# Kernel optimization log

Measured on AMD Instinct MI355X. Metric: run time of the kernel, lower is better.

Reference implementation:

```python
import jax, jax.numpy as jnp
import numpy as np


def setup_inputs() -> dict:
    key = jax.random.key(0)
    k1, = jax.random.split(key, 1)
    b, l, h, w, c = 2, 16, 16, 16, 32
    inputs = jax.random.normal(k1, (b, l, h, w, c), dtype=jnp.float32)
    gamma = jnp.ones((1,), dtype=jnp.float32)
    return {"inputs": inputs, "gamma": gamma}


def reference(inputs, gamma):
    b, l, h, w, c = inputs.shape
    n = l * h * w
    # torch: x = permute->view gives [b, c, n]; here keep [b, n, c] (same memory layout of values)
    xr = inputs.reshape(b, n, c)
    # scores[b,i,j] = sum_c x[b,c,i] * x[b,c,j]
    scores = jnp.einsum('bic,bjc->bij', xr, xr)
    attn = jax.nn.softmax(scores, axis=-1)  # softmax over j (dim=-1)
    # out[b,c,j] = sum_i x[b,c,i] * attn[b,i,j]  ->  [b, n, c] layout
    out = jnp.einsum('bic,bij->bjc', xr, attn)
    out = out.reshape(b, l, h, w, c)
    return out * gamma + inputs
```

## Files before the change

kernel.cpp:

```cpp
#include <hip/hip_runtime.h>


typedef _Float16 half8 __attribute__((ext_vector_type(8)));
typedef _Float16 half4v __attribute__((ext_vector_type(4)));
typedef _Float16 half2v __attribute__((ext_vector_type(2)));
typedef float float4v __attribute__((ext_vector_type(4)));
typedef int int4v __attribute__((ext_vector_type(4)));

#define NN 4096
#define CC 32
#define L2E 1.44269504f
#define SHIFT 48.0f

__global__ __launch_bounds__(256) void k_convert(const float* __restrict__ x,
                                                 _Float16* __restrict__ xf,
                                                 _Float16* __restrict__ xt) {
    const int t = blockIdx.x * 256 + threadIdx.x;
    const int n  = t & 4095;
    const int cg = (t >> 12) & 7;
    const int b  = t >> 15;
    const int row = (b << 12) | n;
    const float4* src = (const float4*)(x + (size_t)row * CC + cg * 4);
    float4 v = *src;
    _Float16 h0 = (_Float16)v.x, h1 = (_Float16)v.y, h2 = (_Float16)v.z, h3 = (_Float16)v.w;
    *(half4v*)(xf + (size_t)row * CC + cg * 4) = (half4v){h0, h1, h2, h3};
    _Float16* p = xt + (size_t)b * CC * NN + (size_t)(n >> 5) * (CC * 32) + cg * 4 * 32 + (n & 31);
    p[0]  = h0;
    p[32] = h1;
    p[64] = h2;
    p[96] = h3;
}

__global__ __launch_bounds__(512, 2) void k_pass1(const _Float16* __restrict__ xf,
                                                  float* __restrict__ c2out) {
    const int tid = threadIdx.x;
    const int wave = tid >> 6, lane = tid & 63;
    const int quad = lane >> 4, l15 = lane & 15;
    const int b = blockIdx.x >> 6;
    const int i0 = (blockIdx.x & 63) * 64;
    const _Float16* xb = xf + (size_t)b * NN * CC;

    const half8 af0 = *(const half8*)(xb + (size_t)(i0 + l15) * CC + quad * 8);
    const half8 af1 = *(const half8*)(xb + (size_t)(i0 + 16 + l15) * CC + quad * 8);
    const half8 af2 = *(const half8*)(xb + (size_t)(i0 + 32 + l15) * CC + quad * 8);
    const half8 af3 = *(const half8*)(xb + (size_t)(i0 + 48 + l15) * CC + quad * 8);
    const float4v zf = {0.f, 0.f, 0.f, 0.f};
    float z0[4] = {0.f, 0.f, 0.f, 0.f};
    float z1[4] = {0.f, 0.f, 0.f, 0.f};
    float z2[4] = {0.f, 0.f, 0.f, 0.f};
    float z3[4] = {0.f, 0.f, 0.f, 0.f};
    const float c2c = -SHIFT * L2E;

    const int jbase = wave * 512;
    half8 b0 = *(const half8*)(xb + (size_t)(jbase + l15) * CC + quad * 8);
    half8 b1 = *(const half8*)(xb + (size_t)(jbase + 16 + l15) * CC + quad * 8);
    half8 b2 = *(const half8*)(xb + (size_t)(jbase + 32 + l15) * CC + quad * 8);
    half8 b3 = *(const half8*)(xb + (size_t)(jbase + 48 + l15) * CC + quad * 8);

    for (int jt = 0; jt < 8; ++jt) {
        const int jn = jbase + ((jt + 1) & 7) * 64;
        half8 n0 = *(const half8*)(xb + (size_t)(jn + l15) * CC + quad * 8);
        half8 n1 = *(const half8*)(xb + (size_t)(jn + 16 + l15) * CC + quad * 8);
        half8 n2 = *(const half8*)(xb + (size_t)(jn + 32 + l15) * CC + quad * 8);
        half8 n3 = *(const half8*)(xb + (size_t)(jn + 48 + l15) * CC + quad * 8);

        {
            float4v s00 = __builtin_amdgcn_mfma_f32_16x16x32_f16(af0, b0, zf, 0, 0, 0);
            float4v s01 = __builtin_amdgcn_mfma_f32_16x16x32_f16(af0, b1, zf, 0, 0, 0);
            float4v s02 = __builtin_amdgcn_mfma_f32_16x16x32_f16(af0, b2, zf, 0, 0, 0);
            float4v s03 = __builtin_amdgcn_mfma_f32_16x16x32_f16(af0, b3, zf, 0, 0, 0);
            float4v s10 = __builtin_amdgcn_mfma_f32_16x16x32_f16(af1, b0, zf, 0, 0, 0);
            float4v s11 = __builtin_amdgcn_mfma_f32_16x16x32_f16(af1, b1, zf, 0, 0, 0);
            float4v s12 = __builtin_amdgcn_mfma_f32_16x16x32_f16(af1, b2, zf, 0, 0, 0);
            float4v s13 = __builtin_amdgcn_mfma_f32_16x16x32_f16(af1, b3, zf, 0, 0, 0);
#pragma unroll
            for (int r = 0; r < 4; ++r) {
                z0[r] += __builtin_amdgcn_exp2f(fmaf(s00[r], L2E, c2c));
                z0[r] += __builtin_amdgcn_exp2f(fmaf(s01[r], L2E, c2c));
                z0[r] += __builtin_amdgcn_exp2f(fmaf(s02[r], L2E, c2c));
                z0[r] += __builtin_amdgcn_exp2f(fmaf(s03[r], L2E, c2c));
                z1[r] += __builtin_amdgcn_exp2f(fmaf(s10[r], L2E, c2c));
                z1[r] += __builtin_amdgcn_exp2f(fmaf(s11[r], L2E, c2c));
                z1[r] += __builtin_amdgcn_exp2f(fmaf(s12[r], L2E, c2c));
                z1[r] += __builtin_amdgcn_exp2f(fmaf(s13[r], L2E, c2c));
            }
        }
        {
            float4v s00 = __builtin_amdgcn_mfma_f32_16x16x32_f16(af2, b0, zf, 0, 0, 0);
            float4v s01 = __builtin_amdgcn_mfma_f32_16x16x32_f16(af2, b1, zf, 0, 0, 0);
            float4v s02 = __builtin_amdgcn_mfma_f32_16x16x32_f16(af2, b2, zf, 0, 0, 0);
            float4v s03 = __builtin_amdgcn_mfma_f32_16x16x32_f16(af2, b3, zf, 0, 0, 0);
            float4v s10 = __builtin_amdgcn_mfma_f32_16x16x32_f16(af3, b0, zf, 0, 0, 0);
            float4v s11 = __builtin_amdgcn_mfma_f32_16x16x32_f16(af3, b1, zf, 0, 0, 0);
            float4v s12 = __builtin_amdgcn_mfma_f32_16x16x32_f16(af3, b2, zf, 0, 0, 0);
            float4v s13 = __builtin_amdgcn_mfma_f32_16x16x32_f16(af3, b3, zf, 0, 0, 0);
#pragma unroll
            for (int r = 0; r < 4; ++r) {
                z2[r] += __builtin_amdgcn_exp2f(fmaf(s00[r], L2E, c2c));
                z2[r] += __builtin_amdgcn_exp2f(fmaf(s01[r], L2E, c2c));
                z2[r] += __builtin_amdgcn_exp2f(fmaf(s02[r], L2E, c2c));
                z2[r] += __builtin_amdgcn_exp2f(fmaf(s03[r], L2E, c2c));
                z3[r] += __builtin_amdgcn_exp2f(fmaf(s10[r], L2E, c2c));
                z3[r] += __builtin_amdgcn_exp2f(fmaf(s11[r], L2E, c2c));
                z3[r] += __builtin_amdgcn_exp2f(fmaf(s12[r], L2E, c2c));
                z3[r] += __builtin_amdgcn_exp2f(fmaf(s13[r], L2E, c2c));
            }
        }
        b0 = n0; b1 = n1; b2 = n2; b3 = n3;
    }
#pragma unroll
    for (int off = 1; off <= 8; off <<= 1) {
#pragma unroll
        for (int r = 0; r < 4; ++r) {
            z0[r] += __shfl_xor(z0[r], off, 64);
            z1[r] += __shfl_xor(z1[r], off, 64);
            z2[r] += __shfl_xor(z2[r], off, 64);
            z3[r] += __shfl_xor(z3[r], off, 64);
        }
    }
    __shared__ float zw[8][64];
    if (l15 == 0) {
#pragma unroll
        for (int r = 0; r < 4; ++r) {
            zw[wave][quad * 4 + r]      = z0[r];
            zw[wave][16 + quad * 4 + r] = z1[r];
            zw[wave][32 + quad * 4 + r] = z2[r];
            zw[wave][48 + quad * 4 + r] = z3[r];
        }
    }
    __syncthreads();
    if (tid < 64) {
        float zs = 0.f;
#pragma unroll
        for (int w = 0; w < 8; ++w) zs += zw[w][tid];
        c2out[b * NN + i0 + tid] = -(__builtin_amdgcn_logf(zs) + SHIFT * L2E);
    }
}

__global__ __launch_bounds__(512, 2) void k_pass2(const _Float16* __restrict__ xf,
                                                  const _Float16* __restrict__ xt,
                                                  const float* __restrict__ c2,
                                                  const float* __restrict__ x,
                                                  const float* __restrict__ gamma,
                                                  float* __restrict__ out) {
    const int tid = threadIdx.x;
    const int wave = tid >> 6, lane = tid & 63;
    const int quad = lane >> 4, l15 = lane & 15;
    const int b = blockIdx.x >> 6;
    const int j0 = (blockIdx.x & 63) * 64;
    const _Float16* xb  = xf + (size_t)b * NN * CC;
    const _Float16* xtb = xt + (size_t)b * CC * NN;
    const float* c2b = c2 + b * NN;

    __shared__ float red[8][64][32];

    const int addrLo = (((quad & 1) << 5) + l15) << 2;
    const int addrHi = addrLo + 64;
    const bool lo32 = (lane < 32);

    const half8 bj0 = *(const half8*)(xb + (size_t)(j0 + l15) * CC + quad * 8);
    const half8 bj1 = *(const half8*)(xb + (size_t)(j0 + 16 + l15) * CC + quad * 8);
    const half8 bj2 = *(const half8*)(xb + (size_t)(j0 + 32 + l15) * CC + quad * 8);
    const half8 bj3 = *(const half8*)(xb + (size_t)(j0 + 48 + l15) * CC + quad * 8);
    const float4v zf = {0.f, 0.f, 0.f, 0.f};
    float4v acc00 = zf, acc01 = zf, acc10 = zf, acc11 = zf;
    float4v acc20 = zf, acc21 = zf, acc30 = zf, acc31 = zf;

    const int ibase = wave * 512;
    half8 a0  = *(const half8*)(xb + (size_t)(ibase + l15) * CC + quad * 8);
    half8 a1  = *(const half8*)(xb + (size_t)(ibase + 16 + l15) * CC + quad * 8);
    half8 xb0 = *(const half8*)(xtb + (size_t)ibase * 32 + l15 * 32 + quad * 8);
    half8 xb1 = *(const half8*)(xtb + (size_t)ibase * 32 + 512 + l15 * 32 + quad * 8);
    float4v c20 = *(const float4v*)(c2b + ibase + quad * 4);
    float4v c21 = *(const float4v*)(c2b + ibase + 16 + quad * 4);

    for (int it = 0; it < 16; ++it) {
        const int inx = ibase + ((it + 1) & 15) * 32;
        half8 na0  = *(const half8*)(xb + (size_t)(inx + l15) * CC + quad * 8);
        half8 na1  = *(const half8*)(xb + (size_t)(inx + 16 + l15) * CC + quad * 8);
        half8 nxb0 = *(const half8*)(xtb + (size_t)inx * 32 + l15 * 32 + quad * 8);
        half8 nxb1 = *(const half8*)(xtb + (size_t)inx * 32 + 512 + l15 * 32 + quad * 8);
        float4v nc20 = *(const float4v*)(c2b + inx + quad * 4);
        float4v nc21 = *(const float4v*)(c2b + inx + 16 + quad * 4);

        {
            float4v s00 = __builtin_amdgcn_mfma_f32_16x16x32_f16(a0, bj0, zf, 0, 0, 0);
            float4v s10 = __builtin_amdgcn_mfma_f32_16x16x32_f16(a1, bj0, zf, 0, 0, 0);
            float4v s01 = __builtin_amdgcn_mfma_f32_16x16x32_f16(a0, bj1, zf, 0, 0, 0);
            float4v s11 = __builtin_amdgcn_mfma_f32_16x16x32_f16(a1, bj1, zf, 0, 0, 0);
            float4v e00, e10, e01, e11;
#pragma unroll
            for (int r = 0; r < 4; ++r) {
                e00[r] = __builtin_amdgcn_exp2f(fmaf(s00[r], L2E, c20[r]));
                e10[r] = __builtin_amdgcn_exp2f(fmaf(s10[r], L2E, c21[r]));
                e01[r] = __builtin_amdgcn_exp2f(fmaf(s01[r], L2E, c20[r]));
                e11[r] = __builtin_amdgcn_exp2f(fmaf(s11[r], L2E, c21[r]));
            }
            {
                const int d0 = __builtin_bit_cast(int, (half2v)__builtin_amdgcn_cvt_pkrtz(e00[0], e00[1]));
                const int d1 = __builtin_bit_cast(int, (half2v)__builtin_amdgcn_cvt_pkrtz(e00[2], e00[3]));
                const int d2 = __builtin_bit_cast(int, (half2v)__builtin_amdgcn_cvt_pkrtz(e10[0], e10[1]));
                const int d3 = __builtin_bit_cast(int, (half2v)__builtin_amdgcn_cvt_pkrtz(e10[2], e10[3]));
                const int q0 = __builtin_amdgcn_ds_bpermute(addrLo, d0);
                const int q1 = __builtin_amdgcn_ds_bpermute(addrLo, d1);
                const int q2 = __builtin_amdgcn_ds_bpermute(addrHi, d0);
                const int q3 = __builtin_amdgcn_ds_bpermute(addrHi, d1);
                const int q4 = __builtin_amdgcn_ds_bpermute(addrLo, d2);
                const int q5 = __builtin_amdgcn_ds_bpermute(addrLo, d3);
                const int q6 = __builtin_amdgcn_ds_bpermute(addrHi, d2);
                const int q7 = __builtin_amdgcn_ds_bpermute(addrHi, d3);
                int4v ai;
                ai[0] = lo32 ? q0 : q4;
                ai[1] = lo32 ? q1 : q5;
                ai[2] = lo32 ? q2 : q6;
                ai[3] = lo32 ? q3 : q7;
                const half8 a2 = __builtin_bit_cast(half8, ai);
                acc00 = __builtin_amdgcn_mfma_f32_16x16x32_f16(a2, xb0, acc00, 0, 0, 0);
                acc01 = __builtin_amdgcn_mfma_f32_16x16x32_f16(a2, xb1, acc01, 0, 0, 0);
            }
            {
                const int d0 = __builtin_bit_cast(int, (half2v)__builtin_amdgcn_cvt_pkrtz(e01[0], e01[1]));
                const int d1 = __builtin_bit_cast(int, (half2v)__builtin_amdgcn_cvt_pkrtz(e01[2], e01[3]));
                const int d2 = __builtin_bit_cast(int, (half2v)__builtin_amdgcn_cvt_pkrtz(e11[0], e11[1]));
                const int d3 = __builtin_bit_cast(int, (half2v)__builtin_amdgcn_cvt_pkrtz(e11[2], e11[3]));
                const int q0 = __builtin_amdgcn_ds_bpermute(addrLo, d0);
                const int q1 = __builtin_amdgcn_ds_bpermute(addrLo, d1);
                const int q2 = __builtin_amdgcn_ds_bpermute(addrHi, d0);
                const int q3 = __builtin_amdgcn_ds_bpermute(addrHi, d1);
                const int q4 = __builtin_amdgcn_ds_bpermute(addrLo, d2);
                const int q5 = __builtin_amdgcn_ds_bpermute(addrLo, d3);
                const int q6 = __builtin_amdgcn_ds_bpermute(addrHi, d2);
                const int q7 = __builtin_amdgcn_ds_bpermute(addrHi, d3);
                int4v ai;
                ai[0] = lo32 ? q0 : q4;
                ai[1] = lo32 ? q1 : q5;
                ai[2] = lo32 ? q2 : q6;
                ai[3] = lo32 ? q3 : q7;
                const half8 a2 = __builtin_bit_cast(half8, ai);
                acc10 = __builtin_amdgcn_mfma_f32_16x16x32_f16(a2, xb0, acc10, 0, 0, 0);
                acc11 = __builtin_amdgcn_mfma_f32_16x16x32_f16(a2, xb1, acc11, 0, 0, 0);
            }
        }
        {
            float4v s00 = __builtin_amdgcn_mfma_f32_16x16x32_f16(a0, bj2, zf, 0, 0, 0);
            float4v s10 = __builtin_amdgcn_mfma_f32_16x16x32_f16(a1, bj2, zf, 0, 0, 0);
            float4v s01 = __builtin_amdgcn_mfma_f32_16x16x32_f16(a0, bj3, zf, 0, 0, 0);
            float4v s11 = __builtin_amdgcn_mfma_f32_16x16x32_f16(a1, bj3, zf, 0, 0, 0);
            float4v e00, e10, e01, e11;
#pragma unroll
            for (int r = 0; r < 4; ++r) {
                e00[r] = __builtin_amdgcn_exp2f(fmaf(s00[r], L2E, c20[r]));
                e10[r] = __builtin_amdgcn_exp2f(fmaf(s10[r], L2E, c21[r]));
                e01[r] = __builtin_amdgcn_exp2f(fmaf(s01[r], L2E, c20[r]));
                e11[r] = __builtin_amdgcn_exp2f(fmaf(s11[r], L2E, c21[r]));
            }
            {
                const int d0 = __builtin_bit_cast(int, (half2v)__builtin_amdgcn_cvt_pkrtz(e00[0], e00[1]));
                const int d1 = __builtin_bit_cast(int, (half2v)__builtin_amdgcn_cvt_pkrtz(e00[2], e00[3]));
                const int d2 = __builtin_bit_cast(int, (half2v)__builtin_amdgcn_cvt_pkrtz(e10[0], e10[1]));
                const int d3 = __builtin_bit_cast(int, (half2v)__builtin_amdgcn_cvt_pkrtz(e10[2], e10[3]));
                const int q0 = __builtin_amdgcn_ds_bpermute(addrLo, d0);
                const int q1 = __builtin_amdgcn_ds_bpermute(addrLo, d1);
                const int q2 = __builtin_amdgcn_ds_bpermute(addrHi, d0);
                const int q3 = __builtin_amdgcn_ds_bpermute(addrHi, d1);
                const int q4 = __builtin_amdgcn_ds_bpermute(addrLo, d2);
                const int q5 = __builtin_amdgcn_ds_bpermute(addrLo, d3);
                const int q6 = __builtin_amdgcn_ds_bpermute(addrHi, d2);
                const int q7 = __builtin_amdgcn_ds_bpermute(addrHi, d3);
                int4v ai;
                ai[0] = lo32 ? q0 : q4;
                ai[1] = lo32 ? q1 : q5;
                ai[2] = lo32 ? q2 : q6;
                ai[3] = lo32 ? q3 : q7;
                const half8 a2 = __builtin_bit_cast(half8, ai);
                acc20 = __builtin_amdgcn_mfma_f32_16x16x32_f16(a2, xb0, acc20, 0, 0, 0);
                acc21 = __builtin_amdgcn_mfma_f32_16x16x32_f16(a2, xb1, acc21, 0, 0, 0);
            }
            {
                const int d0 = __builtin_bit_cast(int, (half2v)__builtin_amdgcn_cvt_pkrtz(e01[0], e01[1]));
                const int d1 = __builtin_bit_cast(int, (half2v)__builtin_amdgcn_cvt_pkrtz(e01[2], e01[3]));
                const int d2 = __builtin_bit_cast(int, (half2v)__builtin_amdgcn_cvt_pkrtz(e11[0], e11[1]));
                const int d3 = __builtin_bit_cast(int, (half2v)__builtin_amdgcn_cvt_pkrtz(e11[2], e11[3]));
                const int q0 = __builtin_amdgcn_ds_bpermute(addrLo, d0);
                const int q1 = __builtin_amdgcn_ds_bpermute(addrLo, d1);
                const int q2 = __builtin_amdgcn_ds_bpermute(addrHi, d0);
                const int q3 = __builtin_amdgcn_ds_bpermute(addrHi, d1);
                const int q4 = __builtin_amdgcn_ds_bpermute(addrLo, d2);
                const int q5 = __builtin_amdgcn_ds_bpermute(addrLo, d3);
                const int q6 = __builtin_amdgcn_ds_bpermute(addrHi, d2);
                const int q7 = __builtin_amdgcn_ds_bpermute(addrHi, d3);
                int4v ai;
                ai[0] = lo32 ? q0 : q4;
                ai[1] = lo32 ? q1 : q5;
                ai[2] = lo32 ? q2 : q6;
                ai[3] = lo32 ? q3 : q7;
                const half8 a2 = __builtin_bit_cast(half8, ai);
                acc30 = __builtin_amdgcn_mfma_f32_16x16x32_f16(a2, xb0, acc30, 0, 0, 0);
                acc31 = __builtin_amdgcn_mfma_f32_16x16x32_f16(a2, xb1, acc31, 0, 0, 0);
            }
        }

        a0 = na0; a1 = na1; xb0 = nxb0; xb1 = nxb1; c20 = nc20; c21 = nc21;
    }

#pragma unroll
    for (int r = 0; r < 4; ++r) {
        red[wave][quad * 4 + r][l15]           = acc00[r];
        red[wave][quad * 4 + r][l15 + 16]      = acc01[r];
        red[wave][16 + quad * 4 + r][l15]      = acc10[r];
        red[wave][16 + quad * 4 + r][l15 + 16] = acc11[r];
        red[wave][32 + quad * 4 + r][l15]      = acc20[r];
        red[wave][32 + quad * 4 + r][l15 + 16] = acc21[r];
        red[wave][48 + quad * 4 + r][l15]      = acc30[r];
        red[wave][48 + quad * 4 + r][l15 + 16] = acc31[r];
    }
    __syncthreads();
    {
        const int jj = tid >> 5, c = tid & 31;
        const float g = gamma[0];
#pragma unroll
        for (int h = 0; h < 4; ++h) {
            const int j = jj + h * 16;
            float s = 0.f;
#pragma unroll
            for (int w = 0; w < 8; ++w) s += red[w][j][c];
            const size_t o = (size_t)(b * NN + j0 + j) * CC + c;
            out[o] = fmaf(g, s, x[o]);
        }
    }
}

extern "C" void kernel_launch(void* const* d_in, const int* in_sizes, int n_in,
                              void* d_out, int out_size, void* d_ws, size_t ws_size,
                              hipStream_t stream) {
    const float* x     = (const float*)d_in[0];
    const float* gamma = (const float*)d_in[1];
    float* out = (float*)d_out;

    _Float16* xf = (_Float16*)d_ws;
    _Float16* xt = xf + (size_t)2 * NN * CC;
    float*    c2 = (float*)(xt + (size_t)2 * CC * NN);

    k_convert<<<dim3(256), dim3(256), 0, stream>>>(x, xf, xt);
    k_pass1 <<<dim3(128), dim3(512), 0, stream>>>(xf, c2);
    k_pass2 <<<dim3(128), dim3(512), 0, stream>>>(xf, xt, c2, x, gamma, out);
}
```

Baseline: 87.49 us.

## Double grid size by splitting query rows in pass1 and i-range in pass2

Pass1 now gives each block 32 query rows instead of 64, doubling its grid to 256 blocks. Pass2 splits the i-reduction into two halves across 256 blocks and combines the partial outputs with float atomicAdd into an output zeroed by the convert kernel, with the residual added by one half only. The aim is to fill more of the GPU's compute units, since 128 blocks underuse the device. The cost is atomic traffic, an extra zeroing write, and a summation order that depends on atomic timing.

```diff
diff --git a/kernel.cpp b/kernel.cpp
--- a/kernel.cpp
+++ b/kernel.cpp
@@ -14,7 +14,8 @@
 
 __global__ __launch_bounds__(256) void k_convert(const float* __restrict__ x,
                                                  _Float16* __restrict__ xf,
-                                                 _Float16* __restrict__ xt) {
+                                                 _Float16* __restrict__ xt,
+                                                 float* __restrict__ out) {
     const int t = blockIdx.x * 256 + threadIdx.x;
     const int n  = t & 4095;
     const int cg = (t >> 12) & 7;
@@ -29,6 +30,7 @@
     p[32] = h1;
     p[64] = h2;
     p[96] = h3;
+    *(float4*)(out + (size_t)t * 4) = (float4){0.f, 0.f, 0.f, 0.f};
 }
 
 __global__ __launch_bounds__(512, 2) void k_pass1(const _Float16* __restrict__ xf,
@@ -36,19 +38,15 @@
     const int tid = threadIdx.x;
     const int wave = tid >> 6, lane = tid & 63;
     const int quad = lane >> 4, l15 = lane & 15;
-    const int b = blockIdx.x >> 6;
-    const int i0 = (blockIdx.x & 63) * 64;
+    const int b = blockIdx.x >> 7;
+    const int i0 = (blockIdx.x & 127) * 32;
     const _Float16* xb = xf + (size_t)b * NN * CC;
 
     const half8 af0 = *(const half8*)(xb + (size_t)(i0 + l15) * CC + quad * 8);
     const half8 af1 = *(const half8*)(xb + (size_t)(i0 + 16 + l15) * CC + quad * 8);
-    const half8 af2 = *(const half8*)(xb + (size_t)(i0 + 32 + l15) * CC + quad * 8);
-    const half8 af3 = *(const half8*)(xb + (size_t)(i0 + 48 + l15) * CC + quad * 8);
     const float4v zf = {0.f, 0.f, 0.f, 0.f};
     float z0[4] = {0.f, 0.f, 0.f, 0.f};
     float z1[4] = {0.f, 0.f, 0.f, 0.f};
-    float z2[4] = {0.f, 0.f, 0.f, 0.f};
-    float z3[4] = {0.f, 0.f, 0.f, 0.f};
     const float c2c = -SHIFT * L2E;
 
     const int jbase = wave * 512;
@@ -64,47 +62,24 @@
         half8 n2 = *(const half8*)(xb + (size_t)(jn + 32 + l15) * CC + quad * 8);
         half8 n3 = *(const half8*)(xb + (size_t)(jn + 48 + l15) * CC + quad * 8);
 
-        {
-            float4v s00 = __builtin_amdgcn_mfma_f32_16x16x32_f16(af0, b0, zf, 0, 0, 0);
-            float4v s01 = __builtin_amdgcn_mfma_f32_16x16x32_f16(af0, b1, zf, 0, 0, 0);
-            float4v s02 = __builtin_amdgcn_mfma_f32_16x16x32_f16(af0, b2, zf, 0, 0, 0);
-            float4v s03 = __builtin_amdgcn_mfma_f32_16x16x32_f16(af0, b3, zf, 0, 0, 0);
-            float4v s10 = __builtin_amdgcn_mfma_f32_16x16x32_f16(af1, b0, zf, 0, 0, 0);
-            float4v s11 = __builtin_amdgcn_mfma_f32_16x16x32_f16(af1, b1, zf, 0, 0, 0);
-            float4v s12 = __builtin_amdgcn_mfma_f32_16x16x32_f16(af1, b2, zf, 0, 0, 0);
-            float4v s13 = __builtin_amdgcn_mfma_f32_16x16x32_f16(af1, b3, zf, 0, 0, 0);
-#pragma unroll
-            for (int r = 0; r < 4; ++r) {
-                z0[r] += __builtin_amdgcn_exp2f(fmaf(s00[r], L2E, c2c));
-                z0[r] += __builtin_amdgcn_exp2f(fmaf(s01[r], L2E, c2c));
-                z0[r] += __builtin_amdgcn_exp2f(fmaf(s02[r], L2E, c2c));
-                z0[r] += __builtin_amdgcn_exp2f(fmaf(s03[r], L2E, c2c));
-                z1[r] += __builtin_amdgcn_exp2f(fmaf(s10[r], L2E, c2c));
-                z1[r] += __builtin_amdgcn_exp2f(fmaf(s11[r], L2E, c2c));
-                z1[r] += __builtin_amdgcn_exp2f(fmaf(s12[r], L2E, c2c));
-                z1[r] += __builtin_amdgcn_exp2f(fmaf(s13[r], L2E, c2c));
-            }
-        }
-        {
-            float4v s00 = __builtin_amdgcn_mfma_f32_16x16x32_f16(af2, b0, zf, 0, 0, 0);
-            float4v s01 = __builtin_amdgcn_mfma_f32_16x16x32_f16(af2, b1, zf, 0, 0, 0);
-            float4v s02 = __builtin_amdgcn_mfma_f32_16x16x32_f16(af2, b2, zf, 0, 0, 0);
-            float4v s03 = __builtin_amdgcn_mfma_f32_16x16x32_f16(af2, b3, zf, 0, 0, 0);
-            float4v s10 = __builtin_amdgcn_mfma_f32_16x16x32_f16(af3, b0, zf, 0, 0, 0);
-            float4v s11 = __builtin_amdgcn_mfma_f32_16x16x32_f16(af3, b1, zf, 0, 0, 0);
-            float4v s12 = __builtin_amdgcn_mfma_f32_16x16x32_f16(af3, b2, zf, 0, 0, 0);
-            float4v s13 = __builtin_amdgcn_mfma_f32_16x16x32_f16(af3, b3, zf, 0, 0, 0);
-#pragma unroll
-            for (int r = 0; r < 4; ++r) {
-                z2[r] += __builtin_amdgcn_exp2f(fmaf(s00[r], L2E, c2c));
-                z2[r] += __builtin_amdgcn_exp2f(fmaf(s01[r], L2E, c2c));
-                z2[r] += __builtin_amdgcn_exp2f(fmaf(s02[r], L2E, c2c));
-                z2[r] += __builtin_amdgcn_exp2f(fmaf(s03[r], L2E, c2c));
-                z3[r] += __builtin_amdgcn_exp2f(fmaf(s10[r], L2E, c2c));
-                z3[r] += __builtin_amdgcn_exp2f(fmaf(s11[r], L2E, c2c));
-                z3[r] += __builtin_amdgcn_exp2f(fmaf(s12[r], L2E, c2c));
-                z3[r] += __builtin_amdgcn_exp2f(fmaf(s13[r], L2E, c2c));
-            }
+        float4v s00 = __builtin_amdgcn_mfma_f32_16x16x32_f16(af0, b0, zf, 0, 0, 0);
+        float4v s01 = __builtin_amdgcn_mfma_f32_16x16x32_f16(af0, b1, zf, 0, 0, 0);
+        float4v s02 = __builtin_amdgcn_mfma_f32_16x16x32_f16(af0, b2, zf, 0, 0, 0);
+        float4v s03 = __builtin_amdgcn_mfma_f32_16x16x32_f16(af0, b3, zf, 0, 0, 0);
+        float4v s10 = __builtin_amdgcn_mfma_f32_16x16x32_f16(af1, b0, zf, 0, 0, 0);
+        float4v s11 = __builtin_amdgcn_mfma_f32_16x16x32_f16(af1, b1, zf, 0, 0, 0);
+        float4v s12 = __builtin_amdgcn_mfma_f32_16x16x32_f16(af1, b2, zf, 0, 0, 0);
+        float4v s13 = __builtin_amdgcn_mfma_f32_16x16x32_f16(af1, b3, zf, 0, 0, 0);
+#pragma unroll
+        for (int r = 0; r < 4; ++r) {
+            z0[r] += __builtin_amdgcn_exp2f(fmaf(s00[r], L2E, c2c));
+            z0[r] += __builtin_amdgcn_exp2f(fmaf(s01[r], L2E, c2c));
+            z0[r] += __builtin_amdgcn_exp2f(fmaf(s02[r], L2E, c2c));
+            z0[r] += __builtin_amdgcn_exp2f(fmaf(s03[r], L2E, c2c));
+            z1[r] += __builtin_amdgcn_exp2f(fmaf(s10[r], L2E, c2c));
+            z1[r] += __builtin_amdgcn_exp2f(fmaf(s11[r], L2E, c2c));
+            z1[r] += __builtin_amdgcn_exp2f(fmaf(s12[r], L2E, c2c));
+            z1[r] += __builtin_amdgcn_exp2f(fmaf(s13[r], L2E, c2c));
         }
         b0 = n0; b1 = n1; b2 = n2; b3 = n3;
     }
@@ -114,22 +89,18 @@
         for (int r = 0; r < 4; ++r) {
             z0[r] += __shfl_xor(z0[r], off, 64);
             z1[r] += __shfl_xor(z1[r], off, 64);
-            z2[r] += __shfl_xor(z2[r], off, 64);
-            z3[r] += __shfl_xor(z3[r], off, 64);
-        }
-    }
-    __shared__ float zw[8][64];
+        }
+    }
+    __shared__ float zw[8][32];
     if (l15 == 0) {
 #pragma unroll
         for (int r = 0; r < 4; ++r) {
             zw[wave][quad * 4 + r]      = z0[r];
             zw[wave][16 + quad * 4 + r] = z1[r];
-            zw[wave][32 + quad * 4 + r] = z2[r];
-            zw[wave][48 + quad * 4 + r] = z3[r];
         }
     }
     __syncthreads();
-    if (tid < 64) {
+    if (tid < 32) {
         float zs = 0.f;
 #pragma unroll
         for (int w = 0; w < 8; ++w) zs += zw[w][tid];
@@ -146,8 +117,9 @@
     const int tid = threadIdx.x;
     const int wave = tid >> 6, lane = tid & 63;
     const int quad = lane >> 4, l15 = lane & 15;
-    const int b = blockIdx.x >> 6;
-    const int j0 = (blockIdx.x & 63) * 64;
+    const int ih = blockIdx.x & 1;
+    const int j0 = ((blockIdx.x >> 1) & 63) * 64;
+    const int b  = blockIdx.x >> 7;
     const _Float16* xb  = xf + (size_t)b * NN * CC;
     const _Float16* xtb = xt + (size_t)b * CC * NN;
     const float* c2b = c2 + b * NN;
@@ -166,20 +138,20 @@
     float4v acc00 = zf, acc01 = zf, acc10 = zf, acc11 = zf;
     float4v acc20 = zf, acc21 = zf, acc30 = zf, acc31 = zf;
 
-    const int ibase = wave * 512;
+    const int ibase = ih * 2048 + wave * 256;
     half8 a0  = *(const half8*)(xb + (size_t)(ibase + l15) * CC + quad * 8);
     half8 a1  = *(const half8*)(xb + (size_t)(ibase + 16 + l15) * CC + quad * 8);
     half8 xb0 = *(const half8*)(xtb + (size_t)ibase * 32 + l15 * 32 + quad * 8);
-    half8 xb1 = *(const half8*)(xtb + (size_t)ibase * 32 + 512 + l15 * 32 + quad * 8);
+    half8 xb1 = *(const half8*)(xtb + (size_t)ibase * 32 + (l15 + 16) * 32 + quad * 8);
     float4v c20 = *(const float4v*)(c2b + ibase + quad * 4);
     float4v c21 = *(const float4v*)(c2b + ibase + 16 + quad * 4);
 
-    for (int it = 0; it < 16; ++it) {
-        const int inx = ibase + ((it + 1) & 15) * 32;
+    for (int it = 0; it < 8; ++it) {
+        const int inx = ibase + ((it + 1) & 7) * 32;
         half8 na0  = *(const half8*)(xb + (size_t)(inx + l15) * CC + quad * 8);
         half8 na1  = *(const half8*)(xb + (size_t)(inx + 16 + l15) * CC + quad * 8);
         half8 nxb0 = *(const half8*)(xtb + (size_t)inx * 32 + l15 * 32 + quad * 8);
-        half8 nxb1 = *(const half8*)(xtb + (size_t)inx * 32 + 512 + l15 * 32 + quad * 8);
+        half8 nxb1 = *(const half8*)(xtb + (size_t)inx * 32 + (l15 + 16) * 32 + quad * 8);
         float4v nc20 = *(const float4v*)(c2b + inx + quad * 4);
         float4v nc21 = *(const float4v*)(c2b + inx + 16 + quad * 4);
 
@@ -325,7 +297,9 @@
 #pragma unroll
             for (int w = 0; w < 8; ++w) s += red[w][j][c];
             const size_t o = (size_t)(b * NN + j0 + j) * CC + c;
-            out[o] = fmaf(g, s, x[o]);
+            float v = g * s;
+            if (ih == 0) v += x[o];
+            atomicAdd(&out[o], v);
         }
     }
 }
@@ -341,7 +315,7 @@
     _Float16* xt = xf + (size_t)2 * NN * CC;
     float*    c2 = (float*)(xt + (size_t)2 * CC * NN);
 
-    k_convert<<<dim3(256), dim3(256), 0, stream>>>(x, xf, xt);
-    k_pass1 <<<dim3(128), dim3(512), 0, stream>>>(xf, c2);
-    k_pass2 <<<dim3(128), dim3(512), 0, stream>>>(xf, xt, c2, x, gamma, out);
+    k_convert<<<dim3(256), dim3(256), 0, stream>>>(x, xf, xt, out);
+    k_pass1 <<<dim3(256), dim3(512), 0, stream>>>(xf, c2);
+    k_pass2 <<<dim3(256), dim3(512), 0, stream>>>(xf, xt, c2, x, gamma, out);
 }
```

Result: faster. 76.57 us (-12.5%).
